# Performance work log

Hardware: AMD Instinct MI355X
Metric: run time of the kernel (lower is better)

Reference implementation:

```python
import jax, jax.numpy as jnp
import numpy as np

TOP_K = 2  # k experts per token


def setup_inputs() -> dict:
    key = jax.random.key(0)
    ks = jax.random.split(key, 6)
    B, L, D, E, F = 2, 2048, 1024, 8, 4096
    x = jax.random.normal(ks[0], (B, L, D), dtype=jnp.float32)
    Wg = jax.random.normal(ks[1], (D, E), dtype=jnp.float32) * (D ** -0.5)
    W1 = jax.random.normal(ks[2], (E, D, F), dtype=jnp.float32) * (D ** -0.5)
    b1 = jnp.zeros((E, F), dtype=jnp.float32)
    W2 = jax.random.normal(ks[3], (E, F, D), dtype=jnp.float32) * (F ** -0.5)
    b2 = jnp.zeros((E, D), dtype=jnp.float32)
    return {"x": x, "Wg": Wg, "W1": W1, "b1": b1, "W2": W2, "b2": b2}


def reference(x, Wg, W1, b1, W2, b2):
    b, l, d = x.shape
    E = Wg.shape[1]
    xt = x.reshape(b * l, d)                      # (N, D)
    N = xt.shape[0]
    # Router: sigmoid gate, top-k (gate weights are NOT renormalized in the source)
    S = jax.nn.sigmoid(xt @ Wg)                   # (N, E)
    G, I = jax.lax.top_k(S, TOP_K)                # (N, k) each
    # Dense equivalent of per-expert gather-MLP-scatter: run every expert
    # on every token, then combine with the sparse top-k routing weights.
    h = jax.nn.gelu(jnp.einsum('nd,edf->enf', xt, W1) + b1[:, None, :])  # (E, N, F)
    y = jnp.einsum('enf,efd->end', h, W2) + b2[:, None, :]               # (E, N, D)
    # combine[n, e] = sum of gate values for slots routed to expert e
    combine = jnp.zeros((N, E), dtype=x.dtype).at[jnp.arange(N)[:, None], I].add(G)
    out = jnp.einsum('ne,end->nd', combine, y)    # (N, D)
    return out.reshape(b, l, d)
```

## Files before the change

kernel.cpp:

```cpp
#include <hip/hip_runtime.h>
#include <math.h>

typedef __bf16 bf16_t;
typedef __attribute__((ext_vector_type(8))) __bf16 bf16x8;
typedef __attribute__((ext_vector_type(4))) __bf16 bf16x4;
typedef __attribute__((ext_vector_type(4))) float f32x4;

#define NTOK 4096
#define DDIM 1024
#define FDIM 4096
#define NEXP 8
#define CAP  4096
#define HROWS (2*NTOK + 128)
#define NPAIR (2*NTOK)
#define MAXB 72

#define PREP_BLOCKS 2048
#define PREP_UNITS 13312

#define GLOAD_LDS16(g, l) \
  __builtin_amdgcn_global_load_lds((__attribute__((address_space(1))) void*)(g), \
                                   (__attribute__((address_space(3))) void*)(l), 16, 0, 0)

__device__ __forceinline__ float fast_gelu(float v) {
  float u = 0.7978845608028654f * (v + 0.044715f * v * v * v);
  float uc = fminf(fmaxf(u, -10.f), 10.f);
  float t = __builtin_amdgcn_exp2f(2.885390081777927f * uc);
  float th = (t - 1.f) * __builtin_amdgcn_rcpf(t + 1.f);
  return 0.5f * v * (1.0f + th);
}

__device__ __forceinline__ void reg_transpose(const float* __restrict__ ip,
                                              bf16_t* __restrict__ op,
                                              int R, int C, int r0, int c0,
                                              int t) {
  const int w = t >> 6;
  const int lane = t & 63;
  const int g = lane >> 4;
  const int m = lane & 15;
  const int rr = r0 + w * 32 + 8 * g;
  const int cc = c0 + 4 * m;
  f32x4 v[8];
#pragma unroll
  for (int ri = 0; ri < 8; ri++)
    v[ri] = *(const f32x4*)(ip + (size_t)(rr + ri) * C + cc);
#pragma unroll
  for (int ci = 0; ci < 4; ci++) {
    bf16x8 o;
#pragma unroll
    for (int ri = 0; ri < 8; ri++) o[ri] = (bf16_t)v[ri][ci];
    *(bf16x8*)(op + (size_t)(cc + ci) * R + rr) = o;
  }
}

__global__ __launch_bounds__(256) void prep_kernel(
    const float* __restrict__ W1, const float* __restrict__ W2,
    const float* __restrict__ x, const float* __restrict__ Wg,
    bf16_t* __restrict__ wt1, bf16_t* __restrict__ wt2,
    bf16_t* __restrict__ xbf, int* __restrict__ tokL, int* __restrict__ cnts,
    int* __restrict__ pairE, int* __restrict__ pairS, float* __restrict__ pairG) {
  const int t = threadIdx.x;
  for (int u = blockIdx.x; u < PREP_UNITS; u += PREP_BLOCKS) {
    if (u < 4096) {
      int e = u >> 9, ti = u & 511;
      int r0 = (ti & 7) * 128, c0 = (ti >> 3) * 64;
      reg_transpose(W1 + (size_t)e * DDIM * FDIM, wt1 + (size_t)e * DDIM * FDIM,
                    DDIM, FDIM, r0, c0, t);
    } else if (u < 8192) {
      int b0 = u - 4096;
      int e = b0 >> 9, ti = b0 & 511;
      int r0 = (ti & 31) * 128, c0 = (ti >> 5) * 64;
      reg_transpose(W2 + (size_t)e * FDIM * DDIM, wt2 + (size_t)e * FDIM * DDIM,
                    FDIM, DDIM, r0, c0, t);
    } else if (u < 12288) {
      int i = (u - 8192) * 256 + t;
      float4 v = ((const float4*)x)[i];
      bf16x4 o;
      o.x = (bf16_t)v.x; o.y = (bf16_t)v.y; o.z = (bf16_t)v.z; o.w = (bf16_t)v.w;
      ((bf16x4*)xbf)[i] = o;
    } else {
      int b0 = u - 12288;
      int wid = t >> 6, lane = t & 63;
      int n = b0 * 4 + wid;
      const float* xr = x + (size_t)n * DDIM;
      double acc[NEXP];
#pragma unroll
      for (int e = 0; e < NEXP; e++) acc[e] = 0.0;
      for (int i = 0; i < DDIM / 64; i++) {
        int d = i * 64 + lane;
        float xv = xr[d];
        const float* wr = Wg + (size_t)d * NEXP;
#pragma unroll
        for (int e = 0; e < NEXP; e++) acc[e] += (double)xv * (double)wr[e];
      }
#pragma unroll
      for (int e = 0; e < NEXP; e++) {
        double v = acc[e];
#pragma unroll
        for (int off = 32; off; off >>= 1) v += __shfl_xor(v, off);
        acc[e] = v;
      }
      if (lane == 0) {
        int i1 = -1, i2 = -1;
        double s1 = -1e300, s2 = -1e300;
#pragma unroll
        for (int e = 0; e < NEXP; e++) {
          double v = acc[e];
          if (v > s1) { s2 = s1; i2 = i1; s1 = v; i1 = e; }
          else if (v > s2) { s2 = v; i2 = e; }
        }
        float g1 = 1.0f / (1.0f + expf((float)(-s1)));
        float g2 = 1.0f / (1.0f + expf((float)(-s2)));
        int p1 = atomicAdd(&cnts[i1], 1);
        tokL[i1 * CAP + p1] = n;
        int p2 = atomicAdd(&cnts[i2], 1);
        tokL[i2 * CAP + p2] = n;
        pairE[2 * n] = i1; pairS[2 * n] = p1; pairG[2 * n] = g1;
        pairE[2 * n + 1] = i2; pairS[2 * n + 1] = p2; pairG[2 * n + 1] = g2;
      }
    }
  }
}

__global__ void offs_kernel(const int* __restrict__ cnts, int* __restrict__ offs,
                            int* __restrict__ blkE, int* __restrict__ blkS) {
  if (threadIdx.x == 0) {
    int s = 0, nb = 0;
    for (int e = 0; e < NEXP; e++) {
      offs[e] = s;
      for (int st = 0; st < cnts[e]; st += 128) { blkE[nb] = e; blkS[nb] = st; nb++; }
      s += cnts[e];
    }
    offs[NEXP] = s;
    for (; nb < MAXB; nb++) { blkE[nb] = NEXP; blkS[nb] = 0; }
  }
}

__global__ __launch_bounds__(256) void gemm1_kernel(
    const bf16_t* __restrict__ xbf, const bf16_t* __restrict__ wt1,
    const float* __restrict__ b1, const int* __restrict__ tokL,
    const int* __restrict__ cnts, const int* __restrict__ offs,
    const int* __restrict__ blkE, const int* __restrict__ blkS,
    bf16_t* __restrict__ H) {
  const int bid = blockIdx.x + 32 * blockIdx.y;
  const int swz = (bid & 7) * 288 + (bid >> 3);
  const int by = swz % 72;
  const int bx = swz / 72;
  const int e = blkE[by];
  if (e >= NEXP) return;
  const int m0 = blkS[by];
  const int cnt = cnts[e];
  const int n0 = bx * 128;
  const int t = threadIdx.x;

  __shared__ alignas(16) bf16_t As[2][128 * 32];
  __shared__ alignas(16) bf16_t Bs[2][128 * 32];

  const int sr = t >> 2;
  const int sc = (t & 3) * 8;
  const int r0 = m0 + sr, r1 = m0 + sr + 64;
  const int tok0 = (r0 < cnt) ? tokL[e * CAP + r0] : 0;
  const int tok1 = (r1 < cnt) ? tokL[e * CAP + r1] : 0;
  const bf16_t* gA0 = xbf + (size_t)tok0 * DDIM + sc;
  const bf16_t* gA1 = xbf + (size_t)tok1 * DDIM + sc;
  const bf16_t* wte = wt1 + (size_t)e * FDIM * DDIM;
  const bf16_t* gB0 = wte + (size_t)(n0 + sr) * DDIM + sc;
  const bf16_t* gB1 = wte + (size_t)(n0 + sr + 64) * DDIM + sc;

  const int lane = t & 63, w = t >> 6;
  const int wm = (w >> 1) * 64, wn = (w & 1) * 64;
  const int lid = lane & 15, quad = lane >> 4;

#define STAGE_G1(buf, kk) do { \
    GLOAD_LDS16(gA0 + (kk), &As[buf][t * 8]); \
    GLOAD_LDS16(gA1 + (kk), &As[buf][2048 + t * 8]); \
    GLOAD_LDS16(gB0 + (kk), &Bs[buf][t * 8]); \
    GLOAD_LDS16(gB1 + (kk), &Bs[buf][2048 + t * 8]); \
  } while (0)

  f32x4 acc[4][4] = {};
  STAGE_G1(0, 0);
  __syncthreads();
  int cur = 0;
  for (int kk = 0; kk < DDIM; kk += 32) {
    if (kk + 32 < DDIM) STAGE_G1(cur ^ 1, kk + 32);
    const bf16_t* Ac = As[cur];
    const bf16_t* Bc = Bs[cur];
    bf16x8 af[4], bfm[4];
#pragma unroll
    for (int i = 0; i < 4; i++)
      af[i] = *(const bf16x8*)(Ac + (wm + i * 16 + lid) * 32 + quad * 8);
#pragma unroll
    for (int j = 0; j < 4; j++)
      bfm[j] = *(const bf16x8*)(Bc + (wn + j * 16 + lid) * 32 + quad * 8);
#pragma unroll
    for (int i = 0; i < 4; i++)
#pragma unroll
      for (int j = 0; j < 4; j++)
        acc[i][j] = __builtin_amdgcn_mfma_f32_16x16x32_bf16(af[i], bfm[j], acc[i][j], 0, 0, 0);
    __syncthreads();
    cur ^= 1;
  }
#undef STAGE_G1

  const float* b1e = b1 + (size_t)e * FDIM;
  const int offe = offs[e];
#pragma unroll
  for (int i = 0; i < 4; i++) {
#pragma unroll
    for (int reg = 0; reg < 4; reg++) {
      int pos = m0 + wm + i * 16 + quad * 4 + reg;
      if (pos >= cnt) continue;
      size_t hrow = (size_t)(offe + pos);
#pragma unroll
      for (int j = 0; j < 4; j++) {
        int col = n0 + wn + j * 16 + lid;
        float v = acc[i][j][reg] + b1e[col];
        H[hrow * FDIM + col] = (bf16_t)fast_gelu(v);
      }
    }
  }
}

__global__ __launch_bounds__(256) void gemm2_kernel(
    const bf16_t* __restrict__ H, const bf16_t* __restrict__ wt2,
    const int* __restrict__ cnts, const int* __restrict__ offs,
    const int* __restrict__ blkE, const int* __restrict__ blkS,
    float* __restrict__ Y0, float* __restrict__ Y1) {
  const int bid = blockIdx.x + 8 * blockIdx.y;
  const int swz = (bid & 7) * 144 + (bid >> 3);
  const int bx = swz & 7;
  const int split = (swz >> 3) & 1;
  const int by = swz >> 4;
  const int e = blkE[by];
  if (e >= NEXP) return;
  const int m0 = blkS[by];
  const int cnt = cnts[e];
  const int n0 = bx * 128;
  const int t = threadIdx.x;
  const int offe = offs[e];
  const int k0 = split * (FDIM / 2);

  __shared__ alignas(16) bf16_t As[2][128 * 32];
  __shared__ alignas(16) bf16_t Bs[2][128 * 32];

  const int sr = t >> 2;
  const int sc = (t & 3) * 8;
  const bf16_t* gA0 = H + (size_t)(offe + m0 + sr) * FDIM + sc + k0;
  const bf16_t* gA1 = H + (size_t)(offe + m0 + sr + 64) * FDIM + sc + k0;
  const bf16_t* wte = wt2 + (size_t)e * DDIM * FDIM;
  const bf16_t* gB0 = wte + (size_t)(n0 + sr) * FDIM + sc + k0;
  const bf16_t* gB1 = wte + (size_t)(n0 + sr + 64) * FDIM + sc + k0;

  const int lane = t & 63, w = t >> 6;
  const int wm = (w >> 1) * 64, wn = (w & 1) * 64;
  const int lid = lane & 15, quad = lane >> 4;

#define STAGE_G2(buf, kk) do { \
    GLOAD_LDS16(gA0 + (kk), &As[buf][t * 8]); \
    GLOAD_LDS16(gA1 + (kk), &As[buf][2048 + t * 8]); \
    GLOAD_LDS16(gB0 + (kk), &Bs[buf][t * 8]); \
    GLOAD_LDS16(gB1 + (kk), &Bs[buf][2048 + t * 8]); \
  } while (0)

  f32x4 acc[4][4] = {};
  STAGE_G2(0, 0);
  __syncthreads();
  int cur = 0;
  for (int kk = 0; kk < FDIM / 2; kk += 32) {
    if (kk + 32 < FDIM / 2) STAGE_G2(cur ^ 1, kk + 32);
    const bf16_t* Ac = As[cur];
    const bf16_t* Bc = Bs[cur];
    bf16x8 af[4], bfm[4];
#pragma unroll
    for (int i = 0; i < 4; i++)
      af[i] = *(const bf16x8*)(Ac + (wm + i * 16 + lid) * 32 + quad * 8);
#pragma unroll
    for (int j = 0; j < 4; j++)
      bfm[j] = *(const bf16x8*)(Bc + (wn + j * 16 + lid) * 32 + quad * 8);
#pragma unroll
    for (int i = 0; i < 4; i++)
#pragma unroll
      for (int j = 0; j < 4; j++)
        acc[i][j] = __builtin_amdgcn_mfma_f32_16x16x32_bf16(af[i], bfm[j], acc[i][j], 0, 0, 0);
    __syncthreads();
    cur ^= 1;
  }
#undef STAGE_G2

  float* Ye = split ? Y1 : Y0;
#pragma unroll
  for (int i = 0; i < 4; i++) {
#pragma unroll
    for (int reg = 0; reg < 4; reg++) {
      int pos = m0 + wm + i * 16 + quad * 4 + reg;
      if (pos >= cnt) continue;
      float* yrow = Ye + (size_t)(offe + pos) * DDIM;
#pragma unroll
      for (int j = 0; j < 4; j++) {
        int col = n0 + wn + j * 16 + lid;
        yrow[col] = acc[i][j][reg];
      }
    }
  }
}

__global__ __launch_bounds__(256) void combine_kernel(
    const float* __restrict__ Y0, const float* __restrict__ Y1,
    const float* __restrict__ b2, const int* __restrict__ pairE,
    const int* __restrict__ pairS, const float* __restrict__ pairG,
    const int* __restrict__ offs, float4* __restrict__ out4) {
  const int n = blockIdx.x;
  const int e1 = pairE[2 * n], e2 = pairE[2 * n + 1];
  const int r1 = offs[e1] + pairS[2 * n];
  const int r2 = offs[e2] + pairS[2 * n + 1];
  const float g1 = pairG[2 * n], g2 = pairG[2 * n + 1];
  const int t = threadIdx.x;
  const float4* ya0 = (const float4*)(Y0 + (size_t)r1 * DDIM);
  const float4* ya1 = (const float4*)(Y1 + (size_t)r1 * DDIM);
  const float4* yb0 = (const float4*)(Y0 + (size_t)r2 * DDIM);
  const float4* yb1 = (const float4*)(Y1 + (size_t)r2 * DDIM);
  const float4* ba = (const float4*)(b2 + (size_t)e1 * DDIM);
  const float4* bb = (const float4*)(b2 + (size_t)e2 * DDIM);
  float4 a0 = ya0[t], a1 = ya1[t], c0 = yb0[t], c1 = yb1[t];
  float4 pa = ba[t], pb = bb[t];
  float4 o;
  o.x = g1 * (a0.x + a1.x + pa.x) + g2 * (c0.x + c1.x + pb.x);
  o.y = g1 * (a0.y + a1.y + pa.y) + g2 * (c0.y + c1.y + pb.y);
  o.z = g1 * (a0.z + a1.z + pa.z) + g2 * (c0.z + c1.z + pb.z);
  o.w = g1 * (a0.w + a1.w + pa.w) + g2 * (c0.w + c1.w + pb.w);
  out4[(size_t)n * (DDIM / 4) + t] = o;
}

extern "C" void kernel_launch(void* const* d_in, const int* in_sizes, int n_in,
                              void* d_out, int out_size, void* d_ws, size_t ws_size,
                              hipStream_t stream) {
  const float* x  = (const float*)d_in[0];
  const float* Wg = (const float*)d_in[1];
  const float* W1 = (const float*)d_in[2];
  const float* b1 = (const float*)d_in[3];
  const float* W2 = (const float*)d_in[4];
  const float* b2 = (const float*)d_in[5];
  float* out = (float*)d_out;

  char* ws = (char*)d_ws;
  size_t off = 0;
  auto alloc = [&](size_t bytes) -> void* {
    void* p = (void*)(ws + off);
    off += (bytes + 255) & ~(size_t)255;
    return p;
  };
  bf16_t* xbf   = (bf16_t*)alloc((size_t)NTOK * DDIM * 2);
  bf16_t* wt1   = (bf16_t*)alloc((size_t)NEXP * FDIM * DDIM * 2);
  bf16_t* wt2   = (bf16_t*)alloc((size_t)NEXP * DDIM * FDIM * 2);
  bf16_t* H     = (bf16_t*)alloc((size_t)HROWS * FDIM * 2);
  int*    tokL  = (int*)alloc((size_t)NEXP * CAP * 4);
  int*    pairE = (int*)alloc((size_t)NPAIR * 4);
  int*    pairS = (int*)alloc((size_t)NPAIR * 4);
  float*  pairG = (float*)alloc((size_t)NPAIR * 4);
  int*    cnts  = (int*)alloc(64);
  int*    offs  = (int*)alloc(64);
  int*    blkE  = (int*)alloc(MAXB * 4);
  int*    blkS  = (int*)alloc(MAXB * 4);
  if (off > ws_size) return;

  float* Y0 = (float*)wt1;
  float* Y1 = Y0 + (size_t)8192 * DDIM;

  hipMemsetAsync(cnts, 0, 64, stream);
  prep_kernel<<<PREP_BLOCKS, 256, 0, stream>>>(W1, W2, x, Wg, wt1, wt2, xbf, tokL,
                                               cnts, pairE, pairS, pairG);
  offs_kernel<<<1, 64, 0, stream>>>(cnts, offs, blkE, blkS);
  gemm1_kernel<<<dim3(FDIM / 128, MAXB), 256, 0, stream>>>(
      xbf, wt1, b1, tokL, cnts, offs, blkE, blkS, H);
  gemm2_kernel<<<dim3(DDIM / 128, MAXB * 2), 256, 0, stream>>>(
      H, wt2, cnts, offs, blkE, blkS, Y0, Y1);
  combine_kernel<<<NTOK, 256, 0, stream>>>(Y0, Y1, b2, pairE, pairS, pairG, offs,
                                           (float4*)out);
}
```

Before: 629.8 us.

## Fuse fp32 weight transpose and bf16 cast into expert GEMM B-tile staging

The separate prep pass that transposed and cast W1 and W2 to bf16 in global memory is removed. Each GEMM now loads the fp32 weights directly into registers, converts and transposes them, and writes a padded, XOR-swizzled B tile into LDS, with the register write deferred until after the MFMAs to overlap with compute. This saves one full read and write of both weight tensors, but the GEMMs now read fp32 weights (twice the bytes) through register staging instead of async global-to-LDS loads, and each weight tile is re-read by every token block of the same expert.

```diff
diff --git a/kernel.cpp b/kernel.cpp
--- a/kernel.cpp
+++ b/kernel.cpp
@@ -15,8 +15,7 @@
 #define NPAIR (2*NTOK)
 #define MAXB 72
 
-#define PREP_BLOCKS 2048
-#define PREP_UNITS 13312
+#define BPAD 40
 
 #define GLOAD_LDS16(g, l) \
   __builtin_amdgcn_global_load_lds((__attribute__((address_space(1))) void*)(g), \
@@ -30,94 +29,80 @@
   return 0.5f * v * (1.0f + th);
 }
 
-__device__ __forceinline__ void reg_transpose(const float* __restrict__ ip,
-                                              bf16_t* __restrict__ op,
-                                              int R, int C, int r0, int c0,
-                                              int t) {
-  const int w = t >> 6;
-  const int lane = t & 63;
-  const int g = lane >> 4;
-  const int m = lane & 15;
-  const int rr = r0 + w * 32 + 8 * g;
-  const int cc = c0 + 4 * m;
-  f32x4 v[8];
-#pragma unroll
-  for (int ri = 0; ri < 8; ri++)
-    v[ri] = *(const f32x4*)(ip + (size_t)(rr + ri) * C + cc);
-#pragma unroll
-  for (int ci = 0; ci < 4; ci++) {
-    bf16x8 o;
-#pragma unroll
-    for (int ri = 0; ri < 8; ri++) o[ri] = (bf16_t)v[ri][ci];
-    *(bf16x8*)(op + (size_t)(cc + ci) * R + rr) = o;
+__device__ __forceinline__ int bswz(int n) {
+  return ((((n >> 1) & 3) ^ ((n >> 2) & 3) ^ ((n >> 4) & 3)) << 1);
+}
+
+__device__ __forceinline__ void bstage_load(const float* __restrict__ p, int ldc,
+                                            f32x4 wr[4]) {
+  wr[0] = *(const f32x4*)(p);
+  wr[1] = *(const f32x4*)(p + ldc);
+  wr[2] = *(const f32x4*)(p + 2 * ldc);
+  wr[3] = *(const f32x4*)(p + 3 * ldc);
+}
+__device__ __forceinline__ void bstage_write(bf16_t* __restrict__ bs, int nb, int kb,
+                                             const f32x4 wr[4]) {
+#pragma unroll
+  for (int j = 0; j < 4; j++) {
+    int n = nb * 4 + j;
+    bf16x4 v;
+    v.x = (bf16_t)wr[0][j]; v.y = (bf16_t)wr[1][j];
+    v.z = (bf16_t)wr[2][j]; v.w = (bf16_t)wr[3][j];
+    *(bf16x4*)(bs + n * BPAD + ((kb ^ bswz(n)) << 2)) = v;
   }
 }
 
 __global__ __launch_bounds__(256) void prep_kernel(
-    const float* __restrict__ W1, const float* __restrict__ W2,
     const float* __restrict__ x, const float* __restrict__ Wg,
-    bf16_t* __restrict__ wt1, bf16_t* __restrict__ wt2,
     bf16_t* __restrict__ xbf, int* __restrict__ tokL, int* __restrict__ cnts,
     int* __restrict__ pairE, int* __restrict__ pairS, float* __restrict__ pairG) {
   const int t = threadIdx.x;
-  for (int u = blockIdx.x; u < PREP_UNITS; u += PREP_BLOCKS) {
-    if (u < 4096) {
-      int e = u >> 9, ti = u & 511;
-      int r0 = (ti & 7) * 128, c0 = (ti >> 3) * 64;
-      reg_transpose(W1 + (size_t)e * DDIM * FDIM, wt1 + (size_t)e * DDIM * FDIM,
-                    DDIM, FDIM, r0, c0, t);
-    } else if (u < 8192) {
-      int b0 = u - 4096;
-      int e = b0 >> 9, ti = b0 & 511;
-      int r0 = (ti & 31) * 128, c0 = (ti >> 5) * 64;
-      reg_transpose(W2 + (size_t)e * FDIM * DDIM, wt2 + (size_t)e * FDIM * DDIM,
-                    FDIM, DDIM, r0, c0, t);
-    } else if (u < 12288) {
-      int i = (u - 8192) * 256 + t;
-      float4 v = ((const float4*)x)[i];
-      bf16x4 o;
-      o.x = (bf16_t)v.x; o.y = (bf16_t)v.y; o.z = (bf16_t)v.z; o.w = (bf16_t)v.w;
-      ((bf16x4*)xbf)[i] = o;
-    } else {
-      int b0 = u - 12288;
-      int wid = t >> 6, lane = t & 63;
-      int n = b0 * 4 + wid;
-      const float* xr = x + (size_t)n * DDIM;
-      double acc[NEXP];
-#pragma unroll
-      for (int e = 0; e < NEXP; e++) acc[e] = 0.0;
-      for (int i = 0; i < DDIM / 64; i++) {
-        int d = i * 64 + lane;
-        float xv = xr[d];
-        const float* wr = Wg + (size_t)d * NEXP;
-#pragma unroll
-        for (int e = 0; e < NEXP; e++) acc[e] += (double)xv * (double)wr[e];
-      }
+#pragma unroll
+  for (int j = 0; j < 4; j++) {
+    int i = (int)(blockIdx.x + j * 1024) * 256 + t;
+    float4 v = ((const float4*)x)[i];
+    bf16x4 o;
+    o.x = (bf16_t)v.x; o.y = (bf16_t)v.y; o.z = (bf16_t)v.z; o.w = (bf16_t)v.w;
+    ((bf16x4*)xbf)[i] = o;
+  }
+  {
+    int wid = t >> 6, lane = t & 63;
+    int n = blockIdx.x * 4 + wid;
+    const float* xr = x + (size_t)n * DDIM;
+    double acc[NEXP];
+#pragma unroll
+    for (int e = 0; e < NEXP; e++) acc[e] = 0.0;
+    for (int i = 0; i < DDIM / 64; i++) {
+      int d = i * 64 + lane;
+      float xv = xr[d];
+      const float* wr = Wg + (size_t)d * NEXP;
+#pragma unroll
+      for (int e = 0; e < NEXP; e++) acc[e] += (double)xv * (double)wr[e];
+    }
+#pragma unroll
+    for (int e = 0; e < NEXP; e++) {
+      double v = acc[e];
+#pragma unroll
+      for (int off = 32; off; off >>= 1) v += __shfl_xor(v, off);
+      acc[e] = v;
+    }
+    if (lane == 0) {
+      int i1 = -1, i2 = -1;
+      double s1 = -1e300, s2 = -1e300;
 #pragma unroll
       for (int e = 0; e < NEXP; e++) {
         double v = acc[e];
-#pragma unroll
-        for (int off = 32; off; off >>= 1) v += __shfl_xor(v, off);
-        acc[e] = v;
+        if (v > s1) { s2 = s1; i2 = i1; s1 = v; i1 = e; }
+        else if (v > s2) { s2 = v; i2 = e; }
       }
-      if (lane == 0) {
-        int i1 = -1, i2 = -1;
-        double s1 = -1e300, s2 = -1e300;
-#pragma unroll
-        for (int e = 0; e < NEXP; e++) {
-          double v = acc[e];
-          if (v > s1) { s2 = s1; i2 = i1; s1 = v; i1 = e; }
-          else if (v > s2) { s2 = v; i2 = e; }
-        }
-        float g1 = 1.0f / (1.0f + expf((float)(-s1)));
-        float g2 = 1.0f / (1.0f + expf((float)(-s2)));
-        int p1 = atomicAdd(&cnts[i1], 1);
-        tokL[i1 * CAP + p1] = n;
-        int p2 = atomicAdd(&cnts[i2], 1);
-        tokL[i2 * CAP + p2] = n;
-        pairE[2 * n] = i1; pairS[2 * n] = p1; pairG[2 * n] = g1;
-        pairE[2 * n + 1] = i2; pairS[2 * n + 1] = p2; pairG[2 * n + 1] = g2;
-      }
+      float g1 = 1.0f / (1.0f + expf((float)(-s1)));
+      float g2 = 1.0f / (1.0f + expf((float)(-s2)));
+      int p1 = atomicAdd(&cnts[i1], 1);
+      tokL[i1 * CAP + p1] = n;
+      int p2 = atomicAdd(&cnts[i2], 1);
+      tokL[i2 * CAP + p2] = n;
+      pairE[2 * n] = i1; pairS[2 * n] = p1; pairG[2 * n] = g1;
+      pairE[2 * n + 1] = i2; pairS[2 * n + 1] = p2; pairG[2 * n + 1] = g2;
     }
   }
 }
@@ -137,7 +122,7 @@
 }
 
 __global__ __launch_bounds__(256) void gemm1_kernel(
-    const bf16_t* __restrict__ xbf, const bf16_t* __restrict__ wt1,
+    const bf16_t* __restrict__ xbf, const float* __restrict__ W1,
     const float* __restrict__ b1, const int* __restrict__ tokL,
     const int* __restrict__ cnts, const int* __restrict__ offs,
     const int* __restrict__ blkE, const int* __restrict__ blkS,
@@ -154,7 +139,7 @@
   const int t = threadIdx.x;
 
   __shared__ alignas(16) bf16_t As[2][128 * 32];
-  __shared__ alignas(16) bf16_t Bs[2][128 * 32];
+  __shared__ alignas(16) bf16_t Bs[2][128 * BPAD];
 
   const int sr = t >> 2;
   const int sc = (t & 3) * 8;
@@ -163,27 +148,31 @@
   const int tok1 = (r1 < cnt) ? tokL[e * CAP + r1] : 0;
   const bf16_t* gA0 = xbf + (size_t)tok0 * DDIM + sc;
   const bf16_t* gA1 = xbf + (size_t)tok1 * DDIM + sc;
-  const bf16_t* wte = wt1 + (size_t)e * FDIM * DDIM;
-  const bf16_t* gB0 = wte + (size_t)(n0 + sr) * DDIM + sc;
-  const bf16_t* gB1 = wte + (size_t)(n0 + sr + 64) * DDIM + sc;
+
+  const int nbt = t & 31, kbt = t >> 5;
+  const float* gW = W1 + (size_t)e * DDIM * FDIM + (size_t)(n0 + nbt * 4);
 
   const int lane = t & 63, w = t >> 6;
   const int wm = (w >> 1) * 64, wn = (w & 1) * 64;
   const int lid = lane & 15, quad = lane >> 4;
 
-#define STAGE_G1(buf, kk) do { \
-    GLOAD_LDS16(gA0 + (kk), &As[buf][t * 8]); \
-    GLOAD_LDS16(gA1 + (kk), &As[buf][2048 + t * 8]); \
-    GLOAD_LDS16(gB0 + (kk), &Bs[buf][t * 8]); \
-    GLOAD_LDS16(gB1 + (kk), &Bs[buf][2048 + t * 8]); \
-  } while (0)
-
+  f32x4 wr[4];
   f32x4 acc[4][4] = {};
-  STAGE_G1(0, 0);
+
+  bstage_load(gW + (size_t)(kbt * 4) * FDIM, FDIM, wr);
+  GLOAD_LDS16(gA0, &As[0][t * 8]);
+  GLOAD_LDS16(gA1, &As[0][2048 + t * 8]);
+  bstage_write(Bs[0], nbt, kbt, wr);
   __syncthreads();
+
   int cur = 0;
   for (int kk = 0; kk < DDIM; kk += 32) {
-    if (kk + 32 < DDIM) STAGE_G1(cur ^ 1, kk + 32);
+    const bool more = (kk + 32 < DDIM);
+    if (more) {
+      bstage_load(gW + (size_t)(kk + 32 + kbt * 4) * FDIM, FDIM, wr);
+      GLOAD_LDS16(gA0 + kk + 32, &As[cur ^ 1][t * 8]);
+      GLOAD_LDS16(gA1 + kk + 32, &As[cur ^ 1][2048 + t * 8]);
+    }
     const bf16_t* Ac = As[cur];
     const bf16_t* Bc = Bs[cur];
     bf16x8 af[4], bfm[4];
@@ -191,17 +180,19 @@
     for (int i = 0; i < 4; i++)
       af[i] = *(const bf16x8*)(Ac + (wm + i * 16 + lid) * 32 + quad * 8);
 #pragma unroll
-    for (int j = 0; j < 4; j++)
-      bfm[j] = *(const bf16x8*)(Bc + (wn + j * 16 + lid) * 32 + quad * 8);
+    for (int j = 0; j < 4; j++) {
+      int n = wn + j * 16 + lid;
+      bfm[j] = *(const bf16x8*)(Bc + n * BPAD + (((2 * quad) ^ bswz(n)) << 2));
+    }
 #pragma unroll
     for (int i = 0; i < 4; i++)
 #pragma unroll
       for (int j = 0; j < 4; j++)
         acc[i][j] = __builtin_amdgcn_mfma_f32_16x16x32_bf16(af[i], bfm[j], acc[i][j], 0, 0, 0);
+    if (more) bstage_write(Bs[cur ^ 1], nbt, kbt, wr);
     __syncthreads();
     cur ^= 1;
   }
-#undef STAGE_G1
 
   const float* b1e = b1 + (size_t)e * FDIM;
   const int offe = offs[e];
@@ -223,7 +214,7 @@
 }
 
 __global__ __launch_bounds__(256) void gemm2_kernel(
-    const bf16_t* __restrict__ H, const bf16_t* __restrict__ wt2,
+    const bf16_t* __restrict__ H, const float* __restrict__ W2,
     const int* __restrict__ cnts, const int* __restrict__ offs,
     const int* __restrict__ blkE, const int* __restrict__ blkS,
     float* __restrict__ Y0, float* __restrict__ Y1) {
@@ -242,33 +233,38 @@
   const int k0 = split * (FDIM / 2);
 
   __shared__ alignas(16) bf16_t As[2][128 * 32];
-  __shared__ alignas(16) bf16_t Bs[2][128 * 32];
+  __shared__ alignas(16) bf16_t Bs[2][128 * BPAD];
 
   const int sr = t >> 2;
   const int sc = (t & 3) * 8;
   const bf16_t* gA0 = H + (size_t)(offe + m0 + sr) * FDIM + sc + k0;
   const bf16_t* gA1 = H + (size_t)(offe + m0 + sr + 64) * FDIM + sc + k0;
-  const bf16_t* wte = wt2 + (size_t)e * DDIM * FDIM;
-  const bf16_t* gB0 = wte + (size_t)(n0 + sr) * FDIM + sc + k0;
-  const bf16_t* gB1 = wte + (size_t)(n0 + sr + 64) * FDIM + sc + k0;
+
+  const int nbt = t & 31, kbt = t >> 5;
+  const float* gW = W2 + (size_t)e * FDIM * DDIM + (size_t)(k0 + kbt * 4) * DDIM
+                    + (size_t)(n0 + nbt * 4);
 
   const int lane = t & 63, w = t >> 6;
   const int wm = (w >> 1) * 64, wn = (w & 1) * 64;
   const int lid = lane & 15, quad = lane >> 4;
 
-#define STAGE_G2(buf, kk) do { \
-    GLOAD_LDS16(gA0 + (kk), &As[buf][t * 8]); \
-    GLOAD_LDS16(gA1 + (kk), &As[buf][2048 + t * 8]); \
-    GLOAD_LDS16(gB0 + (kk), &Bs[buf][t * 8]); \
-    GLOAD_LDS16(gB1 + (kk), &Bs[buf][2048 + t * 8]); \
-  } while (0)
-
+  f32x4 wr[4];
   f32x4 acc[4][4] = {};
-  STAGE_G2(0, 0);
+
+  bstage_load(gW, DDIM, wr);
+  GLOAD_LDS16(gA0, &As[0][t * 8]);
+  GLOAD_LDS16(gA1, &As[0][2048 + t * 8]);
+  bstage_write(Bs[0], nbt, kbt, wr);
   __syncthreads();
+
   int cur = 0;
   for (int kk = 0; kk < FDIM / 2; kk += 32) {
-    if (kk + 32 < FDIM / 2) STAGE_G2(cur ^ 1, kk + 32);
+    const bool more = (kk + 32 < FDIM / 2);
+    if (more) {
+      bstage_load(gW + (size_t)(kk + 32) * DDIM, DDIM, wr);
+      GLOAD_LDS16(gA0 + kk + 32, &As[cur ^ 1][t * 8]);
+      GLOAD_LDS16(gA1 + kk + 32, &As[cur ^ 1][2048 + t * 8]);
+    }
     const bf16_t* Ac = As[cur];
     const bf16_t* Bc = Bs[cur];
     bf16x8 af[4], bfm[4];
@@ -276,17 +272,19 @@
     for (int i = 0; i < 4; i++)
       af[i] = *(const bf16x8*)(Ac + (wm + i * 16 + lid) * 32 + quad * 8);
 #pragma unroll
-    for (int j = 0; j < 4; j++)
-      bfm[j] = *(const bf16x8*)(Bc + (wn + j * 16 + lid) * 32 + quad * 8);
+    for (int j = 0; j < 4; j++) {
+      int n = wn + j * 16 + lid;
+      bfm[j] = *(const bf16x8*)(Bc + n * BPAD + (((2 * quad) ^ bswz(n)) << 2));
+    }
 #pragma unroll
     for (int i = 0; i < 4; i++)
 #pragma unroll
       for (int j = 0; j < 4; j++)
         acc[i][j] = __builtin_amdgcn_mfma_f32_16x16x32_bf16(af[i], bfm[j], acc[i][j], 0, 0, 0);
+    if (more) bstage_write(Bs[cur ^ 1], nbt, kbt, wr);
     __syncthreads();
     cur ^= 1;
   }
-#undef STAGE_G2
 
   float* Ye = split ? Y1 : Y0;
 #pragma unroll
@@ -351,9 +349,9 @@
     return p;
   };
   bf16_t* xbf   = (bf16_t*)alloc((size_t)NTOK * DDIM * 2);
-  bf16_t* wt1   = (bf16_t*)alloc((size_t)NEXP * FDIM * DDIM * 2);
-  bf16_t* wt2   = (bf16_t*)alloc((size_t)NEXP * DDIM * FDIM * 2);
   bf16_t* H     = (bf16_t*)alloc((size_t)HROWS * FDIM * 2);
+  float*  Y0    = (float*)alloc((size_t)2 * NTOK * DDIM * 4);
+  float*  Y1    = (float*)alloc((size_t)2 * NTOK * DDIM * 4);
   int*    tokL  = (int*)alloc((size_t)NEXP * CAP * 4);
   int*    pairE = (int*)alloc((size_t)NPAIR * 4);
   int*    pairS = (int*)alloc((size_t)NPAIR * 4);
@@ -364,17 +362,13 @@
   int*    blkS  = (int*)alloc(MAXB * 4);
   if (off > ws_size) return;
 
-  float* Y0 = (float*)wt1;
-  float* Y1 = Y0 + (size_t)8192 * DDIM;
-
   hipMemsetAsync(cnts, 0, 64, stream);
-  prep_kernel<<<PREP_BLOCKS, 256, 0, stream>>>(W1, W2, x, Wg, wt1, wt2, xbf, tokL,
-                                               cnts, pairE, pairS, pairG);
+  prep_kernel<<<1024, 256, 0, stream>>>(x, Wg, xbf, tokL, cnts, pairE, pairS, pairG);
   offs_kernel<<<1, 64, 0, stream>>>(cnts, offs, blkE, blkS);
   gemm1_kernel<<<dim3(FDIM / 128, MAXB), 256, 0, stream>>>(
-      xbf, wt1, b1, tokL, cnts, offs, blkE, blkS, H);
+      xbf, W1, b1, tokL, cnts, offs, blkE, blkS, H);
   gemm2_kernel<<<dim3(DDIM / 128, MAXB * 2), 256, 0, stream>>>(
-      H, wt2, cnts, offs, blkE, blkS, Y0, Y1);
+      H, W2, cnts, offs, blkE, blkS, Y0, Y1);
   combine_kernel<<<NTOK, 256, 0, stream>>>(Y0, Y1, b2, pairE, pairS, pairG, offs,
                                            (float4*)out);
 }
```

Result: slower. 663.7 us (+5.4%).
